# Kernel optimization log

Hardware: AMD Instinct MI355X
Metric: run time of the kernel (lower is better)

Reference implementation:

```python
import jax, jax.numpy as jnp
import numpy as np

N = 8192
D = 768
TEMPERATURE = 0.1
EPS_NORM = 1e-8   # torch CosineSimilarity eps
EPS_LOG = 1e-6


def setup_inputs() -> dict:
    key = jax.random.key(0)
    k1, k2, k3 = jax.random.split(key, 3)
    features = jax.random.normal(k1, (N, D), dtype=jnp.float32)
    positive_mask = jax.random.randint(k2, (N, N), 0, 2).astype(jnp.float32)
    negative_mask = jax.random.randint(k3, (N, N), 0, 2).astype(jnp.float32)
    return {"features": features, "positive_mask": positive_mask, "negative_mask": negative_mask}


def reference(features, positive_mask, negative_mask):
    n = features.shape[0]
    # cosine similarity: normalize then GEMM (same math as broadcasted CosineSimilarity)
    norms = jnp.linalg.norm(features, axis=1, keepdims=True)
    fn = features / jnp.maximum(norms, EPS_NORM)
    sim = jnp.exp(jnp.matmul(fn, fn.T) / TEMPERATURE)  # [N, N]
    # zero out self-contrast on the diagonal of both masks
    not_eye = 1.0 - jnp.eye(n, dtype=features.dtype)
    pm = positive_mask * not_eye
    nm = negative_mask * not_eye
    pos_sums = pm.sum(axis=1)
    pos_sums = jnp.where(pos_sums == 0, 1.0, pos_sums)
    neg = jnp.sum(sim * nm, axis=1, keepdims=True)  # [N, 1]
    log_prob = -jnp.log(sim / neg + EPS_LOG)        # [N, N]
    per_row = jnp.sum(log_prob * pm, axis=1) / pos_sums
    return jnp.mean(per_row)
```

## Files before the change

kernel.cpp:

```cpp
#include <hip/hip_runtime.h>
#include <hip/hip_bf16.h>

#define NROWS 8192
#define DDIM 768

typedef short short8 __attribute__((ext_vector_type(8)));
typedef float floatx4 __attribute__((ext_vector_type(4)));

__global__ __launch_bounds__(256) void normalize_k(const float* __restrict__ f,
                                                   __hip_bfloat16* __restrict__ fn) {
    const int row = blockIdx.x;
    const int t = threadIdx.x;
    const float* fr = f + (size_t)row * DDIM;
    float v0 = fr[t];
    float v1 = fr[t + 256];
    float v2 = fr[t + 512];
    float ss = v0 * v0 + v1 * v1 + v2 * v2;
#pragma unroll
    for (int m = 32; m; m >>= 1) ss += __shfl_xor(ss, m, 64);
    __shared__ float wsum[4];
    if ((t & 63) == 0) wsum[t >> 6] = ss;
    __syncthreads();
    float tot = wsum[0] + wsum[1] + wsum[2] + wsum[3];
    float inv = 1.0f / fmaxf(sqrtf(tot), 1e-8f);
    __hip_bfloat16* o = fn + (size_t)row * DDIM;
    o[t]       = __float2bfloat16(v0 * inv);
    o[t + 256] = __float2bfloat16(v1 * inv);
    o[t + 512] = __float2bfloat16(v2 * inv);
}

__global__ __launch_bounds__(256, 4) void ntxent_main(
        const __hip_bfloat16* __restrict__ fn,
        const float* __restrict__ pmask, const float* __restrict__ nmask,
        float* __restrict__ negG, float* __restrict__ sG,
        float* __restrict__ pG) {
    __shared__ __hip_bfloat16 Is[128 * 32];
    __shared__ __hip_bfloat16 Js[128 * 32];

    const int t = threadIdx.x;
    const int lane = t & 63;
    const int wv = t >> 6;
    const int wm = wv & 1;
    const int wn = wv >> 1;
    const int q  = lane >> 4;
    const int cl = lane & 15;
    const int rowBase = blockIdx.y * 128;
    const int colBase = blockIdx.x * 128;

    const int rdSw = ((q ^ ((cl >> 1) & 3)) << 4);

    floatx4 acc[4][4];
#pragma unroll
    for (int mf = 0; mf < 4; ++mf)
#pragma unroll
        for (int nf = 0; nf < 4; ++nf)
            acc[mf][nf] = (floatx4){0.f, 0.f, 0.f, 0.f};

    for (int k0 = 0; k0 < DDIM; k0 += 32) {
        __syncthreads();
#pragma unroll
        for (int it = 0; it < 2; ++it) {
            const int s = it * 256 + t;
            const int r = s >> 2;
            const int cg = (s & 3) ^ ((r >> 1) & 3);
            const __hip_bfloat16* ga = fn + (size_t)(rowBase + r) * DDIM + k0 + cg * 8;
            const __hip_bfloat16* gb = fn + (size_t)(colBase + r) * DDIM + k0 + cg * 8;
            __builtin_amdgcn_global_load_lds(
                (const __attribute__((address_space(1))) void*)ga,
                (__attribute__((address_space(3))) void*)((char*)Is + s * 16), 16, 0, 0);
            __builtin_amdgcn_global_load_lds(
                (const __attribute__((address_space(1))) void*)gb,
                (__attribute__((address_space(3))) void*)((char*)Js + s * 16), 16, 0, 0);
        }
        __syncthreads();

        short8 jf[4], if_[4];
#pragma unroll
        for (int mf = 0; mf < 4; ++mf) {
            const int r = wm * 64 + mf * 16 + cl;
            jf[mf] = *(const short8*)((const char*)Js + r * 64 + rdSw);
        }
#pragma unroll
        for (int nf = 0; nf < 4; ++nf) {
            const int r = wn * 64 + nf * 16 + cl;
            if_[nf] = *(const short8*)((const char*)Is + r * 64 + rdSw);
        }
#pragma unroll
        for (int mf = 0; mf < 4; ++mf)
#pragma unroll
            for (int nf = 0; nf < 4; ++nf)
                acc[mf][nf] = __builtin_amdgcn_mfma_f32_16x16x32_bf16(
                    jf[mf], if_[nf], acc[mf][nf], 0, 0, 0);
    }

    const int col64 = colBase + wm * 64;
    const int jb0 = col64 + q * 4;
#pragma unroll
    for (int nf = 0; nf < 4; ++nf) {
        const int grow = rowBase + wn * 64 + nf * 16 + cl;
        const float* prow = pmask + (size_t)grow * NROWS;
        const float* nrow = nmask + (size_t)grow * NROWS;
        float4 pm4[4], nm4[4];
#pragma unroll
        for (int mf = 0; mf < 4; ++mf) {
            pm4[mf] = *(const float4*)(prow + jb0 + mf * 16);
            nm4[mf] = *(const float4*)(nrow + jb0 + mf * 16);
        }
        float aN = 0.f, aS = 0.f, aP = 0.f;
#pragma unroll
        for (int mf = 0; mf < 4; ++mf) {
            const int jbase = jb0 + mf * 16;
#pragma unroll
            for (int reg = 0; reg < 4; ++reg) {
                float pmv = ((const float*)&pm4[mf])[reg];
                float nmv = ((const float*)&nm4[mf])[reg];
                if (grow == jbase + reg) { pmv = 0.f; nmv = 0.f; }
                float v = acc[mf][nf][reg];
                float e = __builtin_amdgcn_exp2f(v * 14.4269504089f);
                aN = fmaf(nmv, e, aN);
                aS = fmaf(pmv, v, aS);
                aP += pmv;
            }
        }
        aN += __shfl_xor(aN, 16, 64);  aN += __shfl_xor(aN, 32, 64);
        aS += __shfl_xor(aS, 16, 64);  aS += __shfl_xor(aS, 32, 64);
        aP += __shfl_xor(aP, 16, 64);  aP += __shfl_xor(aP, 32, 64);
        if (q == 0) {
            atomicAdd(&negG[grow], aN);
            atomicAdd(&sG[grow],   aS);
            atomicAdd(&pG[grow],   aP);
        }
    }
}

__global__ __launch_bounds__(1024) void final_k(const float* __restrict__ negG,
        const float* __restrict__ sG, const float* __restrict__ pG,
        float* __restrict__ out) {
    const int t = threadIdx.x;
    float sum = 0.f;
    for (int i = t; i < NROWS; i += 1024) {
        float P = pG[i];
        if (P > 0.f) {
            sum += (P * logf(negG[i]) - 10.0f * sG[i]) / P;
        }
    }
#pragma unroll
    for (int m = 32; m; m >>= 1) sum += __shfl_xor(sum, m, 64);
    __shared__ float wsum[16];
    if ((t & 63) == 0) wsum[t >> 6] = sum;
    __syncthreads();
    if (t < 16) {
        float v = wsum[t];
#pragma unroll
        for (int m = 8; m; m >>= 1) v += __shfl_xor(v, m, 16);
        if (t == 0) out[0] = v / (float)NROWS;
    }
}

extern "C" void kernel_launch(void* const* d_in, const int* in_sizes, int n_in,
                              void* d_out, int out_size, void* d_ws, size_t ws_size,
                              hipStream_t stream) {
    const float* feat  = (const float*)d_in[0];
    const float* pmask = (const float*)d_in[1];
    const float* nmask = (const float*)d_in[2];
    float* out = (float*)d_out;

    char* ws = (char*)d_ws;
    __hip_bfloat16* fn = (__hip_bfloat16*)ws;
    float* negG = (float*)(ws + 12582912);
    float* sG = negG + NROWS;
    float* pG = sG + NROWS;

    hipMemsetAsync(negG, 0, 3 * NROWS * sizeof(float), stream);

    normalize_k<<<NROWS, 256, 0, stream>>>(feat, fn);

    dim3 grid(64, 64);
    ntxent_main<<<grid, 256, 0, stream>>>(fn, pmask, nmask, negG, sG, pG);

    final_k<<<1, 1024, 0, stream>>>(negG, sG, pG, out);
}
```

Baseline: 605.9 us.

## Exploit Gram matrix symmetry by computing only upper-triangular tiles

Launches 2080 blocks covering only the triangular tile pairs (row tile ≤ column tile) of the symmetric similarity matrix. For off-diagonal tiles the accumulator is also transposed through shared memory, and the transposed mask rows are processed so both row directions get their reductions. This roughly halves the MFMA work, while the mask traffic (the dominant 512MB read) stays the same. It adds a shared-memory transpose stage, extra syncs and a per-block sqrt-based index decode.

```diff
diff --git a/kernel.cpp b/kernel.cpp
--- a/kernel.cpp
+++ b/kernel.cpp
@@ -6,6 +6,7 @@
 
 typedef short short8 __attribute__((ext_vector_type(8)));
 typedef float floatx4 __attribute__((ext_vector_type(4)));
+#define TSTRIDE 132
 
 __global__ __launch_bounds__(256) void normalize_k(const float* __restrict__ f,
                                                    __hip_bfloat16* __restrict__ fn) {
@@ -34,8 +35,10 @@
         const float* __restrict__ pmask, const float* __restrict__ nmask,
         float* __restrict__ negG, float* __restrict__ sG,
         float* __restrict__ pG) {
-    __shared__ __hip_bfloat16 Is[128 * 32];
-    __shared__ __hip_bfloat16 Js[128 * 32];
+    __shared__ __align__(16) char smem[32 * TSTRIDE * 4];
+    __hip_bfloat16* Is = (__hip_bfloat16*)smem;
+    __hip_bfloat16* Js = Is + 128 * 32;
+    float* T = (float*)smem;
 
     const int t = threadIdx.x;
     const int lane = t & 63;
@@ -44,8 +47,15 @@
     const int wn = wv >> 1;
     const int q  = lane >> 4;
     const int cl = lane & 15;
-    const int rowBase = blockIdx.y * 128;
-    const int colBase = blockIdx.x * 128;
+
+    const int bt = blockIdx.x;
+    int r = (int)((sqrtf(8.0f * (float)bt + 1.0f) - 1.0f) * 0.5f);
+    while ((r + 1) * (r + 2) / 2 <= bt) ++r;
+    while (r * (r + 1) / 2 > bt) --r;
+    const int c = bt - r * (r + 1) / 2;
+    const int rowBase = c * 128;
+    const int colBase = r * 128;
+    const bool offDiag = (c != r);
 
     const int rdSw = ((q ^ ((cl >> 1) & 3)) << 4);
 
@@ -61,10 +71,10 @@
 #pragma unroll
         for (int it = 0; it < 2; ++it) {
             const int s = it * 256 + t;
-            const int r = s >> 2;
-            const int cg = (s & 3) ^ ((r >> 1) & 3);
-            const __hip_bfloat16* ga = fn + (size_t)(rowBase + r) * DDIM + k0 + cg * 8;
-            const __hip_bfloat16* gb = fn + (size_t)(colBase + r) * DDIM + k0 + cg * 8;
+            const int rr = s >> 2;
+            const int cg = (s & 3) ^ ((rr >> 1) & 3);
+            const __hip_bfloat16* ga = fn + (size_t)(rowBase + rr) * DDIM + k0 + cg * 8;
+            const __hip_bfloat16* gb = fn + (size_t)(colBase + rr) * DDIM + k0 + cg * 8;
             __builtin_amdgcn_global_load_lds(
                 (const __attribute__((address_space(1))) void*)ga,
                 (__attribute__((address_space(3))) void*)((char*)Is + s * 16), 16, 0, 0);
@@ -77,13 +87,13 @@
         short8 jf[4], if_[4];
 #pragma unroll
         for (int mf = 0; mf < 4; ++mf) {
-            const int r = wm * 64 + mf * 16 + cl;
-            jf[mf] = *(const short8*)((const char*)Js + r * 64 + rdSw);
+            const int rr = wm * 64 + mf * 16 + cl;
+            jf[mf] = *(const short8*)((const char*)Js + rr * 64 + rdSw);
         }
 #pragma unroll
         for (int nf = 0; nf < 4; ++nf) {
-            const int r = wn * 64 + nf * 16 + cl;
-            if_[nf] = *(const short8*)((const char*)Is + r * 64 + rdSw);
+            const int rr = wn * 64 + nf * 16 + cl;
+            if_[nf] = *(const short8*)((const char*)Is + rr * 64 + rdSw);
         }
 #pragma unroll
         for (int mf = 0; mf < 4; ++mf)
@@ -131,6 +141,64 @@
             atomicAdd(&pG[grow],   aP);
         }
     }
+
+    if (offDiag) {
+        const int jl2 = t >> 3;
+        const int iseg = (t & 7) * 16;
+#pragma unroll
+        for (int st = 0; st < 4; ++st) {
+            __syncthreads();
+            if (wm == (st >> 1)) {
+#pragma unroll
+                for (int m2 = 0; m2 < 2; ++m2) {
+                    const int mf = (st & 1) * 2 + m2;
+#pragma unroll
+                    for (int nf = 0; nf < 4; ++nf) {
+                        const int i = wn * 64 + nf * 16 + cl;
+#pragma unroll
+                        for (int reg = 0; reg < 4; ++reg) {
+                            const int jl = m2 * 16 + q * 4 + reg;
+                            T[jl * TSTRIDE + i] = acc[mf][nf][reg];
+                        }
+                    }
+                }
+            }
+            __syncthreads();
+            const int jg = colBase + st * 32 + jl2;
+            const float* prow = pmask + (size_t)jg * NROWS + rowBase + iseg;
+            const float* nrow = nmask + (size_t)jg * NROWS + rowBase + iseg;
+            float4 pm4[4], nm4[4];
+#pragma unroll
+            for (int u = 0; u < 4; ++u) {
+                pm4[u] = *(const float4*)(prow + u * 4);
+                nm4[u] = *(const float4*)(nrow + u * 4);
+            }
+            const float4* tv = (const float4*)(T + jl2 * TSTRIDE + iseg);
+            float aN = 0.f, aS = 0.f, aP = 0.f;
+#pragma unroll
+            for (int u = 0; u < 4; ++u) {
+                float4 v4 = tv[u];
+#pragma unroll
+                for (int e = 0; e < 4; ++e) {
+                    float v = ((const float*)&v4)[e];
+                    float pmv = ((const float*)&pm4[u])[e];
+                    float nmv = ((const float*)&nm4[u])[e];
+                    float ex = __builtin_amdgcn_exp2f(v * 14.4269504089f);
+                    aN = fmaf(nmv, ex, aN);
+                    aS = fmaf(pmv, v, aS);
+                    aP += pmv;
+                }
+            }
+            aN += __shfl_xor(aN, 1, 64); aN += __shfl_xor(aN, 2, 64); aN += __shfl_xor(aN, 4, 64);
+            aS += __shfl_xor(aS, 1, 64); aS += __shfl_xor(aS, 2, 64); aS += __shfl_xor(aS, 4, 64);
+            aP += __shfl_xor(aP, 1, 64); aP += __shfl_xor(aP, 2, 64); aP += __shfl_xor(aP, 4, 64);
+            if ((t & 7) == 0) {
+                atomicAdd(&negG[jg], aN);
+                atomicAdd(&sG[jg],   aS);
+                atomicAdd(&pG[jg],   aP);
+            }
+        }
+    }
 }
 
 __global__ __launch_bounds__(1024) void final_k(const float* __restrict__ negG,
@@ -175,8 +243,7 @@
 
     normalize_k<<<NROWS, 256, 0, stream>>>(feat, fn);
 
-    dim3 grid(64, 64);
-    ntxent_main<<<grid, 256, 0, stream>>>(fn, pmask, nmask, negG, sG, pG);
+    ntxent_main<<<2080, 256, 0, stream>>>(fn, pmask, nmask, negG, sG, pG);
 
     final_k<<<1, 1024, 0, stream>>>(negG, sG, pG, out);
 }
```

After: 586.1 us. 3.3% less time.

## Exploit Gram matrix symmetry by computing only upper-triangular tiles

Applied to the files above, without the earlier changes.

Because fn·fnᵀ is symmetric, the kernel now launches only the 2080 lower/upper triangular 128x128 tiles, decoded from a linear block index. Each off-diagonal tile applies its GEMM result to both the (i,j) masks, read coalesced, and the transposed (j,i) masks, read as strided scalar loads, and accumulates per-column sums with extra shuffles and atomics. This roughly halves the MFMA work, but the transposed mask reads are uncoalesced and mask bandwidth (two 256MB fp32 arrays) still has to be fully read, so the kernel may remain memory-bound.

```diff
diff --git a/kernel.cpp b/kernel.cpp
--- a/kernel.cpp
+++ b/kernel.cpp
@@ -44,8 +44,15 @@
     const int wn = wv >> 1;
     const int q  = lane >> 4;
     const int cl = lane & 15;
-    const int rowBase = blockIdx.y * 128;
-    const int colBase = blockIdx.x * 128;
+
+    const int bt = blockIdx.x;
+    int r = (int)((sqrtf(8.0f * (float)bt + 1.0f) - 1.0f) * 0.5f);
+    while ((r + 1) * (r + 2) / 2 <= bt) ++r;
+    while (r * (r + 1) / 2 > bt) --r;
+    const int c = bt - r * (r + 1) / 2;
+    const int rowBase = c * 128;
+    const int colBase = r * 128;
+    const bool offDiag = (c != r);
 
     const int rdSw = ((q ^ ((cl >> 1) & 3)) << 4);
 
@@ -61,10 +68,10 @@
 #pragma unroll
         for (int it = 0; it < 2; ++it) {
             const int s = it * 256 + t;
-            const int r = s >> 2;
-            const int cg = (s & 3) ^ ((r >> 1) & 3);
-            const __hip_bfloat16* ga = fn + (size_t)(rowBase + r) * DDIM + k0 + cg * 8;
-            const __hip_bfloat16* gb = fn + (size_t)(colBase + r) * DDIM + k0 + cg * 8;
+            const int rr = s >> 2;
+            const int cg = (s & 3) ^ ((rr >> 1) & 3);
+            const __hip_bfloat16* ga = fn + (size_t)(rowBase + rr) * DDIM + k0 + cg * 8;
+            const __hip_bfloat16* gb = fn + (size_t)(colBase + rr) * DDIM + k0 + cg * 8;
             __builtin_amdgcn_global_load_lds(
                 (const __attribute__((address_space(1))) void*)ga,
                 (__attribute__((address_space(3))) void*)((char*)Is + s * 16), 16, 0, 0);
@@ -77,13 +84,13 @@
         short8 jf[4], if_[4];
 #pragma unroll
         for (int mf = 0; mf < 4; ++mf) {
-            const int r = wm * 64 + mf * 16 + cl;
-            jf[mf] = *(const short8*)((const char*)Js + r * 64 + rdSw);
+            const int rr = wm * 64 + mf * 16 + cl;
+            jf[mf] = *(const short8*)((const char*)Js + rr * 64 + rdSw);
         }
 #pragma unroll
         for (int nf = 0; nf < 4; ++nf) {
-            const int r = wn * 64 + nf * 16 + cl;
-            if_[nf] = *(const short8*)((const char*)Is + r * 64 + rdSw);
+            const int rr = wn * 64 + nf * 16 + cl;
+            if_[nf] = *(const short8*)((const char*)Is + rr * 64 + rdSw);
         }
 #pragma unroll
         for (int mf = 0; mf < 4; ++mf)
@@ -95,40 +102,82 @@
 
     const int col64 = colBase + wm * 64;
     const int jb0 = col64 + q * 4;
+    const int ibase = rowBase + wn * 64;
+
+    float dN[4], dS[4], dP[4];
+#pragma unroll
+    for (int nf = 0; nf < 4; ++nf) { dN[nf] = 0.f; dS[nf] = 0.f; dP[nf] = 0.f; }
+
+#pragma unroll
+    for (int mf = 0; mf < 4; ++mf) {
+        const int jbase = jb0 + mf * 16;
+        float mN[4], mS[4], mP[4];
+#pragma unroll
+        for (int g = 0; g < 4; ++g) { mN[g] = 0.f; mS[g] = 0.f; mP[g] = 0.f; }
+
+#pragma unroll
+        for (int nf = 0; nf < 4; ++nf) {
+            const int grow = ibase + nf * 16 + cl;
+            float4 pd = *(const float4*)(pmask + (size_t)grow * NROWS + jbase);
+            float4 nd = *(const float4*)(nmask + (size_t)grow * NROWS + jbase);
+            float pmm[4], nmm[4];
+            if (offDiag) {
+#pragma unroll
+                for (int g = 0; g < 4; ++g) {
+                    const size_t mo = (size_t)(jbase + g) * NROWS + grow;
+                    pmm[g] = pmask[mo];
+                    nmm[g] = nmask[mo];
+                }
+            }
+#pragma unroll
+            for (int g = 0; g < 4; ++g) {
+                float pdv = ((const float*)&pd)[g];
+                float ndv = ((const float*)&nd)[g];
+                if (!offDiag && grow == jbase + g) { pdv = 0.f; ndv = 0.f; }
+                float v = acc[mf][nf][g];
+                float e = __builtin_amdgcn_exp2f(v * 14.4269504089f);
+                dN[nf] = fmaf(ndv, e, dN[nf]);
+                dS[nf] = fmaf(pdv, v, dS[nf]);
+                dP[nf] += pdv;
+                if (offDiag) {
+                    mN[g] = fmaf(nmm[g], e, mN[g]);
+                    mS[g] = fmaf(pmm[g], v, mS[g]);
+                    mP[g] += pmm[g];
+                }
+            }
+        }
+        if (offDiag) {
+#pragma unroll
+            for (int g = 0; g < 4; ++g) {
+#pragma unroll
+                for (int m = 1; m < 16; m <<= 1) {
+                    mN[g] += __shfl_xor(mN[g], m, 64);
+                    mS[g] += __shfl_xor(mS[g], m, 64);
+                    mP[g] += __shfl_xor(mP[g], m, 64);
+                }
+            }
+            if (cl == 0) {
+#pragma unroll
+                for (int g = 0; g < 4; ++g) {
+                    const int jg = jbase + g;
+                    atomicAdd(&negG[jg], mN[g]);
+                    atomicAdd(&sG[jg],   mS[g]);
+                    atomicAdd(&pG[jg],   mP[g]);
+                }
+            }
+        }
+    }
+
 #pragma unroll
     for (int nf = 0; nf < 4; ++nf) {
-        const int grow = rowBase + wn * 64 + nf * 16 + cl;
-        const float* prow = pmask + (size_t)grow * NROWS;
-        const float* nrow = nmask + (size_t)grow * NROWS;
-        float4 pm4[4], nm4[4];
-#pragma unroll
-        for (int mf = 0; mf < 4; ++mf) {
-            pm4[mf] = *(const float4*)(prow + jb0 + mf * 16);
-            nm4[mf] = *(const float4*)(nrow + jb0 + mf * 16);
-        }
-        float aN = 0.f, aS = 0.f, aP = 0.f;
-#pragma unroll
-        for (int mf = 0; mf < 4; ++mf) {
-            const int jbase = jb0 + mf * 16;
-#pragma unroll
-            for (int reg = 0; reg < 4; ++reg) {
-                float pmv = ((const float*)&pm4[mf])[reg];
-                float nmv = ((const float*)&nm4[mf])[reg];
-                if (grow == jbase + reg) { pmv = 0.f; nmv = 0.f; }
-                float v = acc[mf][nf][reg];
-                float e = __builtin_amdgcn_exp2f(v * 14.4269504089f);
-                aN = fmaf(nmv, e, aN);
-                aS = fmaf(pmv, v, aS);
-                aP += pmv;
-            }
-        }
-        aN += __shfl_xor(aN, 16, 64);  aN += __shfl_xor(aN, 32, 64);
-        aS += __shfl_xor(aS, 16, 64);  aS += __shfl_xor(aS, 32, 64);
-        aP += __shfl_xor(aP, 16, 64);  aP += __shfl_xor(aP, 32, 64);
+        dN[nf] += __shfl_xor(dN[nf], 16, 64);  dN[nf] += __shfl_xor(dN[nf], 32, 64);
+        dS[nf] += __shfl_xor(dS[nf], 16, 64);  dS[nf] += __shfl_xor(dS[nf], 32, 64);
+        dP[nf] += __shfl_xor(dP[nf], 16, 64);  dP[nf] += __shfl_xor(dP[nf], 32, 64);
         if (q == 0) {
-            atomicAdd(&negG[grow], aN);
-            atomicAdd(&sG[grow],   aS);
-            atomicAdd(&pG[grow],   aP);
+            const int grow = ibase + nf * 16 + cl;
+            atomicAdd(&negG[grow], dN[nf]);
+            atomicAdd(&sG[grow],   dS[nf]);
+            atomicAdd(&pG[grow],   dP[nf]);
         }
     }
 }
@@ -175,8 +224,7 @@
 
     normalize_k<<<NROWS, 256, 0, stream>>>(feat, fn);
 
-    dim3 grid(64, 64);
-    ntxent_main<<<grid, 256, 0, stream>>>(fn, pmask, nmask, negG, sG, pG);
+    ntxent_main<<<2080, 256, 0, stream>>>(fn, pmask, nmask, negG, sG, pG);
 
     final_k<<<1, 1024, 0, stream>>>(negG, sG, pG, out);
 }
```

Result: slower. 828.9 us (+36.8%).
